# Optimization experiments

Measured on AMD Instinct MI355X. Metric: run time of the kernel, lower is better.

## Reference

```python
import jax, jax.numpy as jnp
import numpy as np

IN_FEATURES = 4096


def _golay_sequence(n):
    # recursive Shapiro-Rudin / Golay 'a' sequence, truncated to n
    pow2 = 1
    while pow2 < n:
        pow2 *= 2
    a = np.array([1.0], dtype=np.float32)
    b = np.array([1.0], dtype=np.float32)
    k = 1
    while k < pow2:
        a, b = np.concatenate([a, b]), np.concatenate([a, -b])
        k *= 2
    return a[:n]


def fwht(x):
    """Normalized fast Walsh-Hadamard transform over the last axis.
    log2(n) butterfly stages, each scaled by 1/sqrt(2)."""
    shape = x.shape
    n = shape[-1]
    inv_sqrt2 = jnp.asarray(1.0 / np.sqrt(2.0), x.dtype)
    h = 1
    while h < n:
        xr = x.reshape(shape[:-1] + (n // (2 * h), 2, h))
        a = xr[..., 0, :]
        bb = xr[..., 1, :]
        x = (jnp.stack((a + bb, a - bb), axis=-2) * inv_sqrt2).reshape(shape)
        h *= 2
    return x


def _transform_features(x, golay):
    # elementwise Golay sign/scale, then blockwise Hadamard.
    n = x.shape[-1]
    block = 1
    c = 1
    while c <= n:
        if n % c == 0:
            block = c
        c *= 2
    num_blocks = n // block
    xm = (x * golay).reshape(x.shape[:-1] + (num_blocks, block))
    return fwht(xm).reshape(x.shape)


def setup_inputs() -> dict:
    key = jax.random.key(0)
    k1, k2, k3 = jax.random.split(key, 3)
    B, S, D, O = 4, 2048, IN_FEATURES, 4096
    x = jax.random.normal(k1, (B, S, D), dtype=jnp.float32)
    W = jax.random.normal(k2, (O, D), dtype=jnp.float32) * (1.0 / np.sqrt(D))
    b = jax.random.normal(k3, (O,), dtype=jnp.float32) * 0.01
    golay = jnp.asarray(_golay_sequence(D))
    return {"x": x, "golay": golay, "W": W, "b": b}


def reference(x, golay, W, b):
    x_trans = _transform_features(x, golay)
    # norm is Identity (use_rms_norm=False)
    return jnp.einsum('bsd,od->bso', x_trans, W) + b
```

## Files before the change

kernel.cpp:

```cpp
#include <hip/hip_runtime.h>
#include <hip/hip_bf16.h>

typedef __attribute__((ext_vector_type(8))) short short8;
typedef __attribute__((ext_vector_type(4))) float f32x4;

#define D_IN   4096
#define M_TOT  8192
#define N_TOT  4096
#define BM     256
#define BN     256
#define BK     32
#define NT     (D_IN / BK)
#define SLOT_SH 16384

__device__ __forceinline__ unsigned short f2bf(float f) {
  union { float f; unsigned int u; } v; v.f = f;
  unsigned int r = v.u + 0x7fffu + ((v.u >> 16) & 1u);
  return (unsigned short)(r >> 16);
}

__device__ __forceinline__ void async16(const void* gptr, void* lptr) {
  __builtin_amdgcn_global_load_lds(
      (const __attribute__((address_space(1))) void*)gptr,
      (__attribute__((address_space(3))) void*)lptr, 16, 0, 0);
}

__global__ __launch_bounds__(256) void prep_x_kernel(const float* __restrict__ x,
                                                     const float* __restrict__ golay,
                                                     unsigned short* __restrict__ z) {
  size_t i = ((size_t)blockIdx.x * 256 + threadIdx.x) * 4;
  float4 v = *(const float4*)(x + i);
  float4 g = *(const float4*)(golay + (i & (D_IN - 1)));
  union { unsigned short u[4]; uint2 v; } o;
  o.u[0] = f2bf(v.x * g.x);
  o.u[1] = f2bf(v.y * g.y);
  o.u[2] = f2bf(v.z * g.z);
  o.u[3] = f2bf(v.w * g.w);
  *(uint2*)(z + i) = o.v;
}

__device__ __forceinline__ void butterfly16(float v[16]) {
  #pragma unroll
  for (int s = 0; s < 4; ++s) {
    const int h = 1 << s;
    #pragma unroll
    for (int p = 0; p < 8; ++p) {
      const int i = ((p >> s) << (s + 1)) | (p & (h - 1));
      const int j = i | h;
      float a = v[i], b = v[j];
      v[i] = a + b;
      v[j] = a - b;
    }
  }
}

__global__ __launch_bounds__(256) void fwht_w_kernel(const float* __restrict__ W,
                                                     unsigned short* __restrict__ Wt) {
  __shared__ float lds[D_IN];
  const int o = blockIdx.x;
  const int tid = threadIdx.x;
  const int tHi = tid >> 4, tLo = tid & 15;
  float v[16];

  {
    const float4* src = (const float4*)(W + (size_t)o * D_IN + tid * 16);
    #pragma unroll
    for (int q = 0; q < 4; ++q) {
      float4 t = src[q];
      v[q * 4 + 0] = t.x; v[q * 4 + 1] = t.y; v[q * 4 + 2] = t.z; v[q * 4 + 3] = t.w;
    }
  }
  butterfly16(v);
  #pragma unroll
  for (int j = 0; j < 16; ++j) lds[j * 256 + tHi * 16 + tLo] = v[j];
  __syncthreads();

  {
    const float4* src = (const float4*)(lds + tid * 16);
    #pragma unroll
    for (int q = 0; q < 4; ++q) {
      float4 t = src[q];
      v[q * 4 + 0] = t.x; v[q * 4 + 1] = t.y; v[q * 4 + 2] = t.z; v[q * 4 + 3] = t.w;
    }
  }
  butterfly16(v);
  __syncthreads();
  #pragma unroll
  for (int j = 0; j < 16; ++j) lds[j * 256 + tHi * 16 + tLo] = v[j];
  __syncthreads();

  {
    const float4* src = (const float4*)(lds + tid * 16);
    #pragma unroll
    for (int q = 0; q < 4; ++q) {
      float4 t = src[q];
      v[q * 4 + 0] = t.x; v[q * 4 + 1] = t.y; v[q * 4 + 2] = t.z; v[q * 4 + 3] = t.w;
    }
  }
  butterfly16(v);
  unsigned short* dst = Wt + (size_t)o * D_IN;
  #pragma unroll
  for (int j = 0; j < 16; ++j)
    dst[j * 256 + tid] = f2bf(v[j] * 0.015625f);
}

__device__ __forceinline__ void stage_tile(const unsigned short* __restrict__ Z,
                                           const unsigned short* __restrict__ Wt,
                                           unsigned short* lds, int t,
                                           int bm0, int bn0, int w, int ln, int gch) {
  unsigned short* sA = lds + (t & 3) * SLOT_SH;
  unsigned short* sB = sA + 8192;
  const int kof = t * BK + gch * 8;
  #pragma unroll
  for (int l = 0; l < 2; ++l) {
    const int row = w * 32 + l * 16 + (ln >> 2);
    const int dst = w * 1024 + l * 512 + ln * 8;
    async16(Z  + (size_t)(bm0 + row) * D_IN + kof, sA + dst);
    async16(Wt + (size_t)(bn0 + row) * D_IN + kof, sB + dst);
  }
}

__device__ __forceinline__ void compute_tile(const unsigned short* lds, int t,
                                             int abase, int bbase, f32x4 acc[8][4]) {
  const unsigned short* sA = lds + (t & 3) * SLOT_SH + abase;
  const unsigned short* sB = lds + (t & 3) * SLOT_SH + 8192 + bbase;
  short8 a[8], b[4];
  #pragma unroll
  for (int f = 0; f < 8; ++f) a[f] = *(const short8*)(sA + f * 512);
  #pragma unroll
  for (int n = 0; n < 4; ++n) b[n] = *(const short8*)(sB + n * 512);
  __builtin_amdgcn_s_setprio(1);
  #pragma unroll
  for (int f = 0; f < 8; ++f)
    #pragma unroll
    for (int n = 0; n < 4; ++n)
      acc[f][n] = __builtin_amdgcn_mfma_f32_16x16x32_bf16(a[f], b[n], acc[f][n], 0, 0, 0);
  __builtin_amdgcn_s_setprio(0);
}

#define TILE_SYNC(VM)                                        \
  __builtin_amdgcn_sched_barrier(0);                         \
  asm volatile("s_waitcnt lgkmcnt(0)" ::: "memory");         \
  asm volatile("s_waitcnt vmcnt(" #VM ")" ::: "memory");     \
  __builtin_amdgcn_s_barrier();

__global__ __launch_bounds__(512, 2) void gemm_bt_kernel(
    const unsigned short* __restrict__ Z,
    const unsigned short* __restrict__ Wt,
    const float* __restrict__ bias,
    float* __restrict__ C) {
  extern __shared__ unsigned short lds[];

  const int cpx = gridDim.x >> 3;
  const int wg  = ((int)blockIdx.x & 7) * cpx + ((int)blockIdx.x >> 3);
  const int NTN = N_TOT / BN;
  const int bm0 = (wg / NTN) * BM;
  const int bn0 = (wg % NTN) * BN;

  const int tid = threadIdx.x;
  const int w   = tid >> 6;
  const int ln  = tid & 63;
  const int lr  = ln & 15;
  const int ck  = ln >> 4;
  const int wr  = w >> 2;
  const int wc  = w & 3;

  const int gch = (ln & 3) ^ ((ln >> 2) & 3) ^ (ln >> 4);
  const int swz = ck ^ (lr & 3) ^ ((lr >> 2) & 3);
  const int abase = (wr * 128 + lr) * 32 + swz * 8;
  const int bbase = (wc * 64  + lr) * 32 + swz * 8;

  f32x4 acc[8][4] = {};

  stage_tile(Z, Wt, lds, 0, bm0, bn0, w, ln, gch);
  stage_tile(Z, Wt, lds, 1, bm0, bn0, w, ln, gch);
  stage_tile(Z, Wt, lds, 2, bm0, bn0, w, ln, gch);
  asm volatile("s_waitcnt vmcnt(8)" ::: "memory");
  __builtin_amdgcn_s_barrier();

  for (int t = 0; t < NT - 3; ++t) {
    stage_tile(Z, Wt, lds, t + 3, bm0, bn0, w, ln, gch);
    compute_tile(lds, t, abase, bbase, acc);
    TILE_SYNC(8)
  }
  compute_tile(lds, NT - 3, abase, bbase, acc);
  TILE_SYNC(4)
  compute_tile(lds, NT - 2, abase, bbase, acc);
  TILE_SYNC(0)
  compute_tile(lds, NT - 1, abase, bbase, acc);

  const int cm = bm0 + wr * 128;
  const int cn = bn0 + wc * 64 + lr;
  #pragma unroll
  for (int n = 0; n < 4; ++n) {
    const float bv = bias[cn + n * 16];
    #pragma unroll
    for (int f = 0; f < 8; ++f) {
      #pragma unroll
      for (int r = 0; r < 4; ++r) {
        C[(size_t)(cm + f * 16 + ck * 4 + r) * N_TOT + cn + n * 16] = acc[f][n][r] + bv;
      }
    }
  }
}

extern "C" void kernel_launch(void* const* d_in, const int* in_sizes, int n_in,
                              void* d_out, int out_size, void* d_ws, size_t ws_size,
                              hipStream_t stream) {
  const float* x     = (const float*)d_in[0];
  const float* golay = (const float*)d_in[1];
  const float* W     = (const float*)d_in[2];
  const float* bias  = (const float*)d_in[3];
  float* out         = (float*)d_out;

  unsigned short* z  = (unsigned short*)d_ws;
  unsigned short* wt = (unsigned short*)((char*)d_ws + (size_t)M_TOT * D_IN * 2);

  prep_x_kernel<<<(M_TOT * D_IN) / (256 * 4), 256, 0, stream>>>(x, golay, z);
  fwht_w_kernel<<<N_TOT, 256, 0, stream>>>(W, wt);
  gemm_bt_kernel<<<(M_TOT / BM) * (N_TOT / BN), 512, 4 * SLOT_SH * 2, stream>>>(z, wt, bias, out);
}
```

Measured before the change: 529.4 us.

## Retile GEMM to 256x128x64 with 3-stage LDS ring and new swizzle

Changes the GEMM block tile from 256x256x32 to 256x128x64, giving 8 waves of 64x64 per wave instead of 128x64. The LDS pipeline drops from a 4-slot to a 3-slot ring. Loads for the next tile are now issued after the barrier that follows compute, and an XOR swizzle over 8 chunks is added for the 64-wide K rows. The grid doubles, which gives more blocks for load balance, but per-block reuse falls and more global traffic is needed for the same FLOPs.

```diff
diff --git a/kernel.cpp b/kernel.cpp
--- a/kernel.cpp
+++ b/kernel.cpp
@@ -8,10 +8,11 @@
 #define M_TOT  8192
 #define N_TOT  4096
 #define BM     256
-#define BN     256
-#define BK     32
+#define BN     128
+#define BK     64
 #define NT     (D_IN / BK)
-#define SLOT_SH 16384
+#define SLOT_SH 24576
+#define BOFF_B  16384
 
 __device__ __forceinline__ unsigned short f2bf(float f) {
   union { float f; unsigned int u; } v; v.f = f;
@@ -24,6 +25,11 @@
       (const __attribute__((address_space(1))) void*)gptr,
       (__attribute__((address_space(3))) void*)lptr, 16, 0, 0);
 }
+
+#define VMCNT(n) asm volatile("s_waitcnt vmcnt(" #n ")" ::: "memory")
+#define LGKMC(n) asm volatile("s_waitcnt lgkmcnt(" #n ")" ::: "memory")
+#define SBAR()   __builtin_amdgcn_s_barrier()
+#define SCHED0() __builtin_amdgcn_sched_barrier(0)
 
 __global__ __launch_bounds__(256) void prep_x_kernel(const float* __restrict__ x,
                                                      const float* __restrict__ golay,
@@ -104,46 +110,6 @@
     dst[j * 256 + tid] = f2bf(v[j] * 0.015625f);
 }
 
-__device__ __forceinline__ void stage_tile(const unsigned short* __restrict__ Z,
-                                           const unsigned short* __restrict__ Wt,
-                                           unsigned short* lds, int t,
-                                           int bm0, int bn0, int w, int ln, int gch) {
-  unsigned short* sA = lds + (t & 3) * SLOT_SH;
-  unsigned short* sB = sA + 8192;
-  const int kof = t * BK + gch * 8;
-  #pragma unroll
-  for (int l = 0; l < 2; ++l) {
-    const int row = w * 32 + l * 16 + (ln >> 2);
-    const int dst = w * 1024 + l * 512 + ln * 8;
-    async16(Z  + (size_t)(bm0 + row) * D_IN + kof, sA + dst);
-    async16(Wt + (size_t)(bn0 + row) * D_IN + kof, sB + dst);
-  }
-}
-
-__device__ __forceinline__ void compute_tile(const unsigned short* lds, int t,
-                                             int abase, int bbase, f32x4 acc[8][4]) {
-  const unsigned short* sA = lds + (t & 3) * SLOT_SH + abase;
-  const unsigned short* sB = lds + (t & 3) * SLOT_SH + 8192 + bbase;
-  short8 a[8], b[4];
-  #pragma unroll
-  for (int f = 0; f < 8; ++f) a[f] = *(const short8*)(sA + f * 512);
-  #pragma unroll
-  for (int n = 0; n < 4; ++n) b[n] = *(const short8*)(sB + n * 512);
-  __builtin_amdgcn_s_setprio(1);
-  #pragma unroll
-  for (int f = 0; f < 8; ++f)
-    #pragma unroll
-    for (int n = 0; n < 4; ++n)
-      acc[f][n] = __builtin_amdgcn_mfma_f32_16x16x32_bf16(a[f], b[n], acc[f][n], 0, 0, 0);
-  __builtin_amdgcn_s_setprio(0);
-}
-
-#define TILE_SYNC(VM)                                        \
-  __builtin_amdgcn_sched_barrier(0);                         \
-  asm volatile("s_waitcnt lgkmcnt(0)" ::: "memory");         \
-  asm volatile("s_waitcnt vmcnt(" #VM ")" ::: "memory");     \
-  __builtin_amdgcn_s_barrier();
-
 __global__ __launch_bounds__(512, 2) void gemm_bt_kernel(
     const unsigned short* __restrict__ Z,
     const unsigned short* __restrict__ Wt,
@@ -151,51 +117,95 @@
     float* __restrict__ C) {
   extern __shared__ unsigned short lds[];
 
-  const int cpx = gridDim.x >> 3;
+  const int cpx = (int)gridDim.x >> 3;
   const int wg  = ((int)blockIdx.x & 7) * cpx + ((int)blockIdx.x >> 3);
   const int NTN = N_TOT / BN;
   const int bm0 = (wg / NTN) * BM;
   const int bn0 = (wg % NTN) * BN;
 
-  const int tid = threadIdx.x;
+  const int tid = (int)threadIdx.x;
+  const int ln  = tid & 63;
   const int w   = tid >> 6;
-  const int ln  = tid & 63;
   const int lr  = ln & 15;
   const int ck  = ln >> 4;
-  const int wr  = w >> 2;
-  const int wc  = w & 3;
-
-  const int gch = (ln & 3) ^ ((ln >> 2) & 3) ^ (ln >> 4);
-  const int swz = ck ^ (lr & 3) ^ ((lr >> 2) & 3);
-  const int abase = (wr * 128 + lr) * 32 + swz * 8;
-  const int bbase = (wc * 64  + lr) * 32 + swz * 8;
-
-  f32x4 acc[8][4] = {};
-
-  stage_tile(Z, Wt, lds, 0, bm0, bn0, w, ln, gch);
-  stage_tile(Z, Wt, lds, 1, bm0, bn0, w, ln, gch);
-  stage_tile(Z, Wt, lds, 2, bm0, bn0, w, ln, gch);
-  asm volatile("s_waitcnt vmcnt(8)" ::: "memory");
-  __builtin_amdgcn_s_barrier();
-
-  for (int t = 0; t < NT - 3; ++t) {
-    stage_tile(Z, Wt, lds, t + 3, bm0, bn0, w, ln, gch);
-    compute_tile(lds, t, abase, bbase, acc);
-    TILE_SYNC(8)
-  }
-  compute_tile(lds, NT - 3, abase, bbase, acc);
-  TILE_SYNC(4)
-  compute_tile(lds, NT - 2, abase, bbase, acc);
-  TILE_SYNC(0)
-  compute_tile(lds, NT - 1, abase, bbase, acc);
-
-  const int cm = bm0 + wr * 128;
+  const int wr  = w >> 1;
+  const int wc  = w & 1;
+
+  const int koff0 = ((ck     ) ^ (lr & 7)) * 8;
+  const int koff1 = ((4 | ck ) ^ (lr & 7)) * 8;
+
+  const int srow = tid >> 3;
+  const int sc8  = tid & 7;
+  const int sgc  = sc8 ^ (srow & 7);
+
+  f32x4 acc[4][4] = {};
+
+  #define STAGE(so, tt)                                                              \
+    { _Pragma("unroll")                                                              \
+      for (int l = 0; l < 4; ++l) {                                                  \
+        const int row = l * 64 + srow;                                               \
+        async16(Z + (size_t)(bm0 + row) * D_IN + (tt) * 64 + sgc * 8,                \
+                lds + (so) + row * 64 + sc8 * 8);                                    \
+      }                                                                              \
+      _Pragma("unroll")                                                              \
+      for (int l = 0; l < 2; ++l) {                                                  \
+        const int row = l * 64 + srow;                                               \
+        async16(Wt + (size_t)(bn0 + row) * D_IN + (tt) * 64 + sgc * 8,               \
+                lds + (so) + BOFF_B + row * 64 + sc8 * 8);                           \
+      } }
+
+  #define COMPUTE(so)                                                                \
+    { short8 a[4][2], b[4][2];                                                       \
+      _Pragma("unroll")                                                              \
+      for (int f = 0; f < 4; ++f) {                                                  \
+        const int row = wr * 64 + f * 16 + lr;                                       \
+        a[f][0] = *(const short8*)(lds + (so) + row * 64 + koff0);                   \
+        a[f][1] = *(const short8*)(lds + (so) + row * 64 + koff1);                   \
+      }                                                                              \
+      _Pragma("unroll")                                                              \
+      for (int n = 0; n < 4; ++n) {                                                  \
+        const int row = wc * 64 + n * 16 + lr;                                       \
+        b[n][0] = *(const short8*)(lds + (so) + BOFF_B + row * 64 + koff0);          \
+        b[n][1] = *(const short8*)(lds + (so) + BOFF_B + row * 64 + koff1);          \
+      }                                                                              \
+      __builtin_amdgcn_s_setprio(1);                                                 \
+      _Pragma("unroll")                                                              \
+      for (int kk = 0; kk < 2; ++kk)                                                 \
+        { _Pragma("unroll")                                                          \
+          for (int f = 0; f < 4; ++f)                                                \
+            { _Pragma("unroll")                                                      \
+              for (int n = 0; n < 4; ++n)                                            \
+                acc[f][n] = __builtin_amdgcn_mfma_f32_16x16x32_bf16(                 \
+                    a[f][kk], b[n][kk], acc[f][n], 0, 0, 0); } }                     \
+      __builtin_amdgcn_s_setprio(0); }
+
+  STAGE(0, 0)
+  STAGE(SLOT_SH, 1)
+  STAGE(2 * SLOT_SH, 2)
+  VMCNT(12); SBAR();
+
+  int so = 0;
+  for (int t = 0; t <= NT - 4; ++t) {
+    COMPUTE(so)
+    SCHED0(); LGKMC(0); VMCNT(6); SBAR();
+    STAGE(so, t + 3)
+    so = (so == 2 * SLOT_SH) ? 0 : so + SLOT_SH;
+  }
+  COMPUTE(so)
+  so = (so == 2 * SLOT_SH) ? 0 : so + SLOT_SH;
+  VMCNT(6); SBAR();
+  COMPUTE(so)
+  so = (so == 2 * SLOT_SH) ? 0 : so + SLOT_SH;
+  VMCNT(0); SBAR();
+  COMPUTE(so)
+
+  const int cm = bm0 + wr * 64;
   const int cn = bn0 + wc * 64 + lr;
   #pragma unroll
   for (int n = 0; n < 4; ++n) {
     const float bv = bias[cn + n * 16];
     #pragma unroll
-    for (int f = 0; f < 8; ++f) {
+    for (int f = 0; f < 4; ++f) {
       #pragma unroll
       for (int r = 0; r < 4; ++r) {
         C[(size_t)(cm + f * 16 + ck * 4 + r) * N_TOT + cn + n * 16] = acc[f][n][r] + bv;
@@ -218,5 +228,5 @@
 
   prep_x_kernel<<<(M_TOT * D_IN) / (256 * 4), 256, 0, stream>>>(x, golay, z);
   fwht_w_kernel<<<N_TOT, 256, 0, stream>>>(W, wt);
-  gemm_bt_kernel<<<(M_TOT / BM) * (N_TOT / BN), 512, 4 * SLOT_SH * 2, stream>>>(z, wt, bias, out);
-}
+  gemm_bt_kernel<<<(M_TOT / BM) * (N_TOT / BN), 512, 3 * SLOT_SH * 2, stream>>>(z, wt, bias, out);
+}
```

Measured after the change: 545.9 us. +3.1%, slower.
